# Performance work log

Measured on AMD Instinct MI355X. Metric: run time of the kernel, lower is better.

The kernel has to match this reference:

```python
import jax, jax.numpy as jnp
import numpy as np
import math

_PI = math.pi

@jax.custom_vjp
def atan_spike(h):
    # Heaviside forward, ATan surrogate (alpha=2.0) backward
    return (h >= 0).astype(h.dtype)

def _atan_fwd(h):
    return (h >= 0).astype(h.dtype), h

def _atan_bwd(h, g):
    # d/dh [ (1/pi) atan(pi*h) + 1/2 ] = 1 / (1 + (pi*h)^2)
    return (g / (1.0 + (_PI * h) ** 2),)

atan_spike.defvjp(_atan_fwd, _atan_bwd)

def plif_scan(x, alpha, v_th):
    # x: [T, ...]; PLIF: v += alpha*(x - v); spike; hard reset to 0
    a = alpha.reshape(())
    def step(v, xt):
        v = v + a * (xt - v)
        s = atan_spike(v - v_th)
        v = v * (1.0 - s)
        return v, s
    v0 = jnp.zeros_like(x[0])
    _, spikes = jax.lax.scan(step, v0, x)
    return spikes

def setup_inputs() -> dict:
    key = jax.random.key(0)
    k1, k2, k3 = jax.random.split(key, 3)
    T, B, N, D, H = 4, 8, 1024, 512, 2048
    x = jax.random.normal(k1, (T, B, N, D), dtype=jnp.float32)
    W1 = jax.random.normal(k2, (H, D), dtype=jnp.float32) * (1.0 / math.sqrt(D))
    W2 = jax.random.normal(k3, (D, H), dtype=jnp.float32) * (1.0 / math.sqrt(H))
    alpha1 = jnp.full((1,), 0.5, dtype=jnp.float32)  # 1/tau, tau=2.0
    alpha2 = jnp.full((1,), 0.5, dtype=jnp.float32)
    return {"x": x, "W1": W1, "W2": W2, "alpha1": alpha1, "alpha2": alpha2}

def reference(x, W1, W2, alpha1, alpha2):
    V_TH = 1.0
    h = jnp.einsum('tbnd,hd->tbnh', x, W1)      # fc1 (no bias)
    s1 = plif_scan(h, alpha1, V_TH)             # PLIF neuron 1
    y = jnp.einsum('tbnh,dh->tbnd', s1, W2)     # fc2 (no bias)
    s2 = plif_scan(y, alpha2, V_TH)             # PLIF neuron 2
    return s2
```

## Files before the change

### kernel.cpp

```cpp
#include <hip/hip_runtime.h>

#define T_  4
#define BN_ 8192
#define D_  512
#define H_  2048

typedef float f4 __attribute__((ext_vector_type(4)));
typedef float f32x4 __attribute__((ext_vector_type(4)));
typedef _Float16 f16x8 __attribute__((ext_vector_type(8)));

__device__ __forceinline__ void split8(const f4 u0, const f4 u1, f16x8& hi, f16x8& lo) {
#pragma unroll
    for (int i = 0; i < 4; ++i) {
        _Float16 a = (_Float16)u0[i]; hi[i]     = a; lo[i]     = (_Float16)(u0[i] - (float)a);
        _Float16 b = (_Float16)u1[i]; hi[4 + i] = b; lo[4 + i] = (_Float16)(u1[i] - (float)b);
    }
}

__device__ __forceinline__ void spikes4_to_f16(unsigned b, unsigned& lo, unsigned& hi) {
    const unsigned p0 = (b & 0xFFu) | ((b & 0xFF00u) << 8);
    const unsigned p1 = ((b >> 16) & 0xFFu) | ((b >> 8) & 0xFF0000u);
    lo = p0 * 0x3C00u;
    hi = p1 * 0x3C00u;
}

__device__ __forceinline__ void glds16(const void* g, void* l) {
    __builtin_amdgcn_global_load_lds((const __attribute__((address_space(1))) unsigned int*)g,
                                     (__attribute__((address_space(3))) unsigned int*)l, 16, 0, 0);
}

__global__ __launch_bounds__(256)
void k_split(const float* __restrict__ x, _Float16* __restrict__ xs)
{
    const int b   = blockIdx.x;
    const int t   = b & 3;
    const int k0B = (b >> 2) & 15;
    const int bnB = b >> 6;
    const int kg  = threadIdx.x & 3;
    const int row = threadIdx.x >> 2;

    const float* src = x + ((size_t)t * BN_ + bnB * 64 + row) * D_ + k0B * 32 + kg * 8;
    const f4 u0 = *(const f4*)src;
    const f4 u1 = *(const f4*)(src + 4);
    f16x8 hi, lo;
    split8(u0, u1, hi, lo);

    const size_t base = ((size_t)(bnB * 16 + k0B) * 4 + t) * 4096;
    *(f16x8*)&xs[base +        kg * 512 + row * 8] = hi;
    *(f16x8*)&xs[base + 2048 + kg * 512 + row * 8] = lo;
}

__global__ __launch_bounds__(256)
void k_splitW(const float* __restrict__ W1, _Float16* __restrict__ w1s)
{
    const int gid = blockIdx.x * 256 + threadIdx.x;
    const int col = gid & 127;
    const int kg  = (gid >> 7) & 3;
    const int kb  = (gid >> 9) & 15;
    const int h0b = gid >> 13;

    const float* src = W1 + (size_t)(h0b * 128 + col) * D_ + kb * 32 + kg * 8;
    const f4 u0 = *(const f4*)src;
    const f4 u1 = *(const f4*)(src + 4);
    f16x8 hi, lo;
    split8(u0, u1, hi, lo);

    const size_t base = (size_t)(h0b * 16 + kb) * 8192;
    *(f16x8*)&w1s[base +        kg * 1024 + col * 8] = hi;
    *(f16x8*)&w1s[base + 4096 + kg * 1024 + col * 8] = lo;
}

__global__ __launch_bounds__(256, 2)
void k_fc1b(const _Float16* __restrict__ xs, const _Float16* __restrict__ w1s,
            const float* __restrict__ alphap, unsigned char* __restrict__ s1)
{
    __shared__ _Float16 Ab[2][T_][2][4][64][8];

    const int tid  = threadIdx.x;
    const int lane = tid & 63;
    const int w    = tid >> 6;
    const int wr   = (w >> 1) * 32;
    const int wc   = (w & 1) * 64;
    const int bnB  = blockIdx.x;
    const int bn0  = bnB * 64;
    const int h0   = blockIdx.y * 128;

    const int l15 = lane & 15;
    const int kgl = lane >> 4;
    const int lq  = kgl * 4;

    const float a1v = alphap[0];

    f32x4 acc[T_][2][4];
#pragma unroll
    for (int t = 0; t < T_; ++t)
#pragma unroll
        for (int m = 0; m < 2; ++m)
#pragma unroll
            for (int n = 0; n < 4; ++n) acc[t][m][n] = (f32x4){0.f, 0.f, 0.f, 0.f};

    const char* xbase = (const char*)xs + (size_t)bnB * 16 * 32768;
    const _Float16* bl = w1s + (size_t)blockIdx.y * (16 * 8192)
                             + (size_t)kgl * 1024 + (size_t)(wc + l15) * 8;

    f16x8 bc[2][4], bn_[2][4];

    {
        _Float16* lA = &Ab[0][0][0][0][0][0];
#pragma unroll
        for (int i = 0; i < 8; ++i) {
            const int c = i * 4 + w;
            glds16(xbase + c * 1024 + lane * 16, lA + c * 512);
        }
#pragma unroll
        for (int sp = 0; sp < 2; ++sp)
#pragma unroll
            for (int n = 0; n < 4; ++n)
                bc[sp][n] = *(const f16x8*)(bl + sp * 4096 + n * 128);
    }
    __syncthreads();

    int buf = 0;
    for (int kb = 0; kb < 16; ++kb) {
        if (kb < 15) {
            const char* cb = xbase + (size_t)(kb + 1) * 32768;
            _Float16* lA = &Ab[buf ^ 1][0][0][0][0][0];
#pragma unroll
            for (int i = 0; i < 8; ++i) {
                const int c = i * 4 + w;
                glds16(cb + c * 1024 + lane * 16, lA + c * 512);
            }
            const _Float16* bp = bl + (size_t)(kb + 1) * 8192;
#pragma unroll
            for (int sp = 0; sp < 2; ++sp)
#pragma unroll
                for (int n = 0; n < 4; ++n)
                    bn_[sp][n] = *(const f16x8*)(bp + sp * 4096 + n * 128);
        }

#pragma unroll
        for (int t = 0; t < T_; ++t)
#pragma unroll
            for (int m = 0; m < 2; ++m) {
                const f16x8 a0 = *(const f16x8*)&Ab[buf][t][0][kgl][wr + m * 16 + l15][0];
                const f16x8 a1 = *(const f16x8*)&Ab[buf][t][1][kgl][wr + m * 16 + l15][0];
#pragma unroll
                for (int n = 0; n < 4; ++n) {
                    acc[t][m][n] = __builtin_amdgcn_mfma_f32_16x16x32_f16(a0, bc[0][n], acc[t][m][n], 0, 0, 0);
                    acc[t][m][n] = __builtin_amdgcn_mfma_f32_16x16x32_f16(a0, bc[1][n], acc[t][m][n], 0, 0, 0);
                    acc[t][m][n] = __builtin_amdgcn_mfma_f32_16x16x32_f16(a1, bc[0][n], acc[t][m][n], 0, 0, 0);
                }
            }

        __syncthreads();
        if (kb < 15) {
#pragma unroll
            for (int sp = 0; sp < 2; ++sp)
#pragma unroll
                for (int n = 0; n < 4; ++n) bc[sp][n] = bn_[sp][n];
        }
        buf ^= 1;
    }

#pragma unroll
    for (int m = 0; m < 2; ++m)
#pragma unroll
        for (int n = 0; n < 4; ++n)
#pragma unroll
            for (int q = 0; q < 4; ++q) {
                float v = 0.f;
#pragma unroll
                for (int t = 0; t < T_; ++t) {
                    v = v + a1v * (acc[t][m][n][q] - v);
                    const bool sp = (v >= 1.0f);
                    s1[((size_t)t * BN_ + bn0 + wr + m * 16 + lq + q) * H_ +
                       (h0 + wc + n * 16 + l15)] = sp ? (unsigned char)1 : (unsigned char)0;
                    if (sp) v = 0.f;
                }
            }
}

__global__ __launch_bounds__(256, 2)
void k_fc1(const _Float16* __restrict__ xs, const float* __restrict__ W1,
           const float* __restrict__ alphap, unsigned char* __restrict__ s1)
{
    __shared__ _Float16 Ab[T_][2][4][64][8];
    __shared__ _Float16 Bb[2][4][128][8];

    const int tid  = threadIdx.x;
    const int lane = tid & 63;
    const int w    = tid >> 6;
    const int wr   = (w >> 1) * 32;
    const int wc   = (w & 1) * 64;
    const int bnB  = blockIdx.x;
    const int bn0  = bnB * 64;
    const int h0   = blockIdx.y * 128;

    const int l15 = lane & 15;
    const int kgl = lane >> 4;
    const int lq  = kgl * 4;

    const int bcol = tid & 127;
    const int bkh  = tid >> 7;

    const float a1v = alphap[0];

    f32x4 acc[T_][2][4];
#pragma unroll
    for (int t = 0; t < T_; ++t)
#pragma unroll
        for (int m = 0; m < 2; ++m)
#pragma unroll
            for (int n = 0; n < 4; ++n) acc[t][m][n] = (f32x4){0.f, 0.f, 0.f, 0.f};

    const char* xbase = (const char*)xs + (size_t)bnB * 16 * 32768;
    const float* wp0  = W1 + (size_t)(h0 + bcol) * D_ + bkh * 16;

    f4 w0 = *(const f4*)wp0,       w1 = *(const f4*)(wp0 + 4);
    f4 w2 = *(const f4*)(wp0 + 8), w3 = *(const f4*)(wp0 + 12);

    for (int kb = 0; kb < 16; ++kb) {
        __syncthreads();
        const char* cb = xbase + (size_t)kb * 32768;
        _Float16* lA = &Ab[0][0][0][0][0];
#pragma unroll
        for (int i = 0; i < 8; ++i) {
            const int c = i * 4 + w;
            glds16(cb + c * 1024 + lane * 16, lA + c * 512);
        }
        {
            f16x8 hA, lA2, hB, lB;
            split8(w0, w1, hA, lA2); split8(w2, w3, hB, lB);
            *(f16x8*)&Bb[0][2 * bkh][bcol][0]     = hA;
            *(f16x8*)&Bb[0][2 * bkh + 1][bcol][0] = hB;
            *(f16x8*)&Bb[1][2 * bkh][bcol][0]     = lA2;
            *(f16x8*)&Bb[1][2 * bkh + 1][bcol][0] = lB;
        }
        if (kb < 15) {
            const float* wp = wp0 + (kb + 1) * 32;
            w0 = *(const f4*)wp;       w1 = *(const f4*)(wp + 4);
            w2 = *(const f4*)(wp + 8); w3 = *(const f4*)(wp + 12);
        }
        __syncthreads();

        f16x8 bf0[4], bf1[4];
#pragma unroll
        for (int n = 0; n < 4; ++n) {
            bf0[n] = *(const f16x8*)&Bb[0][kgl][wc + n * 16 + l15][0];
            bf1[n] = *(const f16x8*)&Bb[1][kgl][wc + n * 16 + l15][0];
        }
#pragma unroll
        for (int t = 0; t < T_; ++t)
#pragma unroll
            for (int m = 0; m < 2; ++m) {
                const f16x8 a0 = *(const f16x8*)&Ab[t][0][kgl][wr + m * 16 + l15][0];
                const f16x8 a1 = *(const f16x8*)&Ab[t][1][kgl][wr + m * 16 + l15][0];
#pragma unroll
                for (int n = 0; n < 4; ++n) {
                    acc[t][m][n] = __builtin_amdgcn_mfma_f32_16x16x32_f16(a0, bf0[n], acc[t][m][n], 0, 0, 0);
                    acc[t][m][n] = __builtin_amdgcn_mfma_f32_16x16x32_f16(a0, bf1[n], acc[t][m][n], 0, 0, 0);
                    acc[t][m][n] = __builtin_amdgcn_mfma_f32_16x16x32_f16(a1, bf0[n], acc[t][m][n], 0, 0, 0);
                }
            }
    }

#pragma unroll
    for (int m = 0; m < 2; ++m)
#pragma unroll
        for (int n = 0; n < 4; ++n)
#pragma unroll
            for (int q = 0; q < 4; ++q) {
                float v = 0.f;
#pragma unroll
                for (int t = 0; t < T_; ++t) {
                    v = v + a1v * (acc[t][m][n][q] - v);
                    const bool sp = (v >= 1.0f);
                    s1[((size_t)t * BN_ + bn0 + wr + m * 16 + lq + q) * H_ +
                       (h0 + wc + n * 16 + l15)] = sp ? (unsigned char)1 : (unsigned char)0;
                    if (sp) v = 0.f;
                }
            }
}

__global__ __launch_bounds__(256, 2)
void k_fc2(const unsigned char* __restrict__ s1, const float* __restrict__ W2,
           const float* __restrict__ alphap, float* __restrict__ out)
{
    __shared__ _Float16 A2[2][4][4][64][8];
    __shared__ _Float16 B2[2][2][4][128][8];

    const int tid  = threadIdx.x;
    const int lane = tid & 63;
    const int w    = tid >> 6;
    const int wr   = (w >> 1) * 32;
    const int wc   = (w & 1) * 64;
    const int bn0  = blockIdx.x * 64;
    const int d0   = blockIdx.y * 128;

    const int l15 = lane & 15;
    const int kgl = lane >> 4;
    const int lq  = kgl * 4;

    const int bcol = tid & 127;
    const int bkh  = tid >> 7;
    const int at   = tid >> 6;
    const int arow = lane;

    const float a2v = alphap[0];

    f32x4 acc[T_][2][4];
#pragma unroll
    for (int t = 0; t < T_; ++t)
#pragma unroll
        for (int m = 0; m < 2; ++m)
#pragma unroll
            for (int n = 0; n < 4; ++n) acc[t][m][n] = (f32x4){0.f, 0.f, 0.f, 0.f};

    const unsigned char* ap = s1 + ((size_t)at * BN_ + bn0 + arow) * H_;
    const float*         wp0 = W2 + (size_t)(d0 + bcol) * H_ + bkh * 16;

    {
        const uint4 r0 = *(const uint4*)(ap);
        const uint4 r1 = *(const uint4*)(ap + 16);
        unsigned v[8];
        spikes4_to_f16(r0.x, v[0], v[1]); spikes4_to_f16(r0.y, v[2], v[3]);
        spikes4_to_f16(r0.z, v[4], v[5]); spikes4_to_f16(r0.w, v[6], v[7]);
        *(uint4*)&A2[0][at][0][arow][0] = *(const uint4*)&v[0];
        *(uint4*)&A2[0][at][1][arow][0] = *(const uint4*)&v[4];
        spikes4_to_f16(r1.x, v[0], v[1]); spikes4_to_f16(r1.y, v[2], v[3]);
        spikes4_to_f16(r1.z, v[4], v[5]); spikes4_to_f16(r1.w, v[6], v[7]);
        *(uint4*)&A2[0][at][2][arow][0] = *(const uint4*)&v[0];
        *(uint4*)&A2[0][at][3][arow][0] = *(const uint4*)&v[4];

        const f4 w0 = *(const f4*)wp0, w1 = *(const f4*)(wp0 + 4);
        const f4 w2 = *(const f4*)(wp0 + 8), w3 = *(const f4*)(wp0 + 12);
        f16x8 hA, lA, hB, lB;
        split8(w0, w1, hA, lA); split8(w2, w3, hB, lB);
        *(f16x8*)&B2[0][0][2 * bkh][bcol][0]     = hA;
        *(f16x8*)&B2[0][0][2 * bkh + 1][bcol][0] = hB;
        *(f16x8*)&B2[0][1][2 * bkh][bcol][0]     = lA;
        *(f16x8*)&B2[0][1][2 * bkh + 1][bcol][0] = lB;
    }
    __syncthreads();

    int cur = 0;
    for (int kb = 0; kb < 64; ++kb) {
        uint4 r0, r1; f4 w0, w1, w2, w3;
        if (kb < 63) {
            r0 = *(const uint4*)(ap + (kb + 1) * 32);
            r1 = *(const uint4*)(ap + (kb + 1) * 32 + 16);
            const float* wp = wp0 + (kb + 1) * 32;
            w0 = *(const f4*)wp;       w1 = *(const f4*)(wp + 4);
            w2 = *(const f4*)(wp + 8); w3 = *(const f4*)(wp + 12);
        }

        f16x8 bf0[4], bf1[4];
#pragma unroll
        for (int n = 0; n < 4; ++n) {
            bf0[n] = *(const f16x8*)&B2[cur][0][kgl][wc + n * 16 + l15][0];
            bf1[n] = *(const f16x8*)&B2[cur][1][kgl][wc + n * 16 + l15][0];
        }
#pragma unroll
        for (int t = 0; t < T_; ++t)
#pragma unroll
            for (int m = 0; m < 2; ++m) {
                const f16x8 af = *(const f16x8*)&A2[cur][t][kgl][wr + m * 16 + l15][0];
#pragma unroll
                for (int n = 0; n < 4; ++n) {
                    acc[t][m][n] = __builtin_amdgcn_mfma_f32_16x16x32_f16(af, bf0[n], acc[t][m][n], 0, 0, 0);
                    acc[t][m][n] = __builtin_amdgcn_mfma_f32_16x16x32_f16(af, bf1[n], acc[t][m][n], 0, 0, 0);
                }
            }

        if (kb < 63) {
            unsigned v[8];
            spikes4_to_f16(r0.x, v[0], v[1]); spikes4_to_f16(r0.y, v[2], v[3]);
            spikes4_to_f16(r0.z, v[4], v[5]); spikes4_to_f16(r0.w, v[6], v[7]);
            *(uint4*)&A2[cur ^ 1][at][0][arow][0] = *(const uint4*)&v[0];
            *(uint4*)&A2[cur ^ 1][at][1][arow][0] = *(const uint4*)&v[4];
            spikes4_to_f16(r1.x, v[0], v[1]); spikes4_to_f16(r1.y, v[2], v[3]);
            spikes4_to_f16(r1.z, v[4], v[5]); spikes4_to_f16(r1.w, v[6], v[7]);
            *(uint4*)&A2[cur ^ 1][at][2][arow][0] = *(const uint4*)&v[0];
            *(uint4*)&A2[cur ^ 1][at][3][arow][0] = *(const uint4*)&v[4];

            f16x8 hA, lA, hB, lB;
            split8(w0, w1, hA, lA); split8(w2, w3, hB, lB);
            *(f16x8*)&B2[cur ^ 1][0][2 * bkh][bcol][0]     = hA;
            *(f16x8*)&B2[cur ^ 1][0][2 * bkh + 1][bcol][0] = hB;
            *(f16x8*)&B2[cur ^ 1][1][2 * bkh][bcol][0]     = lA;
            *(f16x8*)&B2[cur ^ 1][1][2 * bkh + 1][bcol][0] = lB;
        }
        __syncthreads();
        cur ^= 1;
    }

#pragma unroll
    for (int m = 0; m < 2; ++m)
#pragma unroll
        for (int n = 0; n < 4; ++n)
#pragma unroll
            for (int q = 0; q < 4; ++q) {
                float v = 0.f;
#pragma unroll
                for (int t = 0; t < T_; ++t) {
                    v = v + a2v * (acc[t][m][n][q] - v);
                    const bool sp = (v >= 1.0f);
                    out[((size_t)t * BN_ + bn0 + wr + m * 16 + lq + q) * D_ +
                        (d0 + wc + n * 16 + l15)] = sp ? 1.0f : 0.0f;
                    if (sp) v = 0.f;
                }
            }
}

extern "C" void kernel_launch(void* const* d_in, const int* in_sizes, int n_in,
                              void* d_out, int out_size, void* d_ws, size_t ws_size,
                              hipStream_t stream) {
    const float* x      = (const float*)d_in[0];
    const float* W1     = (const float*)d_in[1];
    const float* W2     = (const float*)d_in[2];
    const float* alpha1 = (const float*)d_in[3];
    const float* alpha2 = (const float*)d_in[4];
    float* out = (float*)d_out;

    unsigned char* s1 = (unsigned char*)d_ws;
    _Float16* xs = (_Float16*)d_out;
    const size_t S1_BYTES = (size_t)T_ * BN_ * H_;
    const size_t W1S_BYTES = (size_t)H_ * D_ * 2 * sizeof(_Float16);

    k_split<<<dim3(8192), dim3(256), 0, stream>>>(x, xs);

    if (ws_size >= S1_BYTES + W1S_BYTES) {
        _Float16* w1s = (_Float16*)((char*)d_ws + S1_BYTES);
        k_splitW<<<dim3(512), dim3(256), 0, stream>>>(W1, w1s);
        k_fc1b<<<dim3(128, 16), dim3(256), 0, stream>>>(xs, w1s, alpha1, s1);
    } else {
        k_fc1<<<dim3(128, 16), dim3(256), 0, stream>>>(xs, W1, alpha1, s1);
    }
    k_fc2<<<dim3(128, 4), dim3(256), 0, stream>>>(s1, W2, alpha2, out);
}
```

Baseline: 304.8 us.

## Swizzle fc1 block order into panels and unroll K loop by two

Launches fc1 as a 1D grid and remaps each block id so that 16 row-blocks sweep all 16 H-tiles inside a 256-block panel. Nearby blocks then share x and W1 tiles in L2. The K loop is also manually unrolled by two with ping-pong register buffers for B, which removes the per-iteration register copy and the buffer-index toggling. The remap assumes exactly 2048 blocks laid out this way.

```diff
diff --git a/kernel.cpp b/kernel.cpp
--- a/kernel.cpp
+++ b/kernel.cpp
@@ -81,9 +81,14 @@
     const int w    = tid >> 6;
     const int wr   = (w >> 1) * 32;
     const int wc   = (w & 1) * 64;
-    const int bnB  = blockIdx.x;
-    const int bn0  = bnB * 64;
-    const int h0   = blockIdx.y * 128;
+
+    const int gid   = blockIdx.x;
+    const int panel = gid >> 8;
+    const int h0i   = (gid >> 4) & 15;
+    const int bnL   = gid & 15;
+    const int bnB   = panel * 16 + bnL;
+    const int bn0   = bnB * 64;
+    const int h0    = h0i * 128;
 
     const int l15 = lane & 15;
     const int kgl = lane >> 4;
@@ -100,66 +105,64 @@
             for (int n = 0; n < 4; ++n) acc[t][m][n] = (f32x4){0.f, 0.f, 0.f, 0.f};
 
     const char* xbase = (const char*)xs + (size_t)bnB * 16 * 32768;
-    const _Float16* bl = w1s + (size_t)blockIdx.y * (16 * 8192)
+    const _Float16* bl = w1s + (size_t)h0i * (16 * 8192)
                              + (size_t)kgl * 1024 + (size_t)(wc + l15) * 8;
 
-    f16x8 bc[2][4], bn_[2][4];
-
-    {
-        _Float16* lA = &Ab[0][0][0][0][0][0];
-#pragma unroll
-        for (int i = 0; i < 8; ++i) {
-            const int c = i * 4 + w;
-            glds16(xbase + c * 1024 + lane * 16, lA + c * 512);
-        }
-#pragma unroll
-        for (int sp = 0; sp < 2; ++sp)
-#pragma unroll
-            for (int n = 0; n < 4; ++n)
-                bc[sp][n] = *(const f16x8*)(bl + sp * 4096 + n * 128);
-    }
+#define FC1_GLDS(BUF, KB)                                                        \
+    {                                                                            \
+        const char* cb_ = xbase + (size_t)(KB) * 32768;                          \
+        _Float16* lA_ = &Ab[BUF][0][0][0][0][0];                                 \
+        _Pragma("unroll")                                                        \
+        for (int i_ = 0; i_ < 8; ++i_) {                                         \
+            const int c_ = i_ * 4 + w;                                           \
+            glds16(cb_ + c_ * 1024 + lane * 16, lA_ + c_ * 512);                 \
+        }                                                                        \
+    }
+
+#define FC1_BLOAD(KB, B0, B1)                                                    \
+    {                                                                            \
+        const _Float16* bp_ = bl + (size_t)(KB) * 8192;                          \
+        _Pragma("unroll")                                                        \
+        for (int n_ = 0; n_ < 4; ++n_) {                                         \
+            B0[n_] = *(const f16x8*)(bp_ + n_ * 128);                            \
+            B1[n_] = *(const f16x8*)(bp_ + 4096 + n_ * 128);                     \
+        }                                                                        \
+    }
+
+#define FC1_COMPUTE(BUF, B0, B1)                                                 \
+    _Pragma("unroll")                                                            \
+    for (int t_ = 0; t_ < T_; ++t_)                                              \
+        _Pragma("unroll")                                                        \
+        for (int m_ = 0; m_ < 2; ++m_) {                                         \
+            const f16x8 a0_ = *(const f16x8*)&Ab[BUF][t_][0][kgl][wr + m_ * 16 + l15][0]; \
+            const f16x8 a1_ = *(const f16x8*)&Ab[BUF][t_][1][kgl][wr + m_ * 16 + l15][0]; \
+            _Pragma("unroll")                                                    \
+            for (int n_ = 0; n_ < 4; ++n_) {                                     \
+                acc[t_][m_][n_] = __builtin_amdgcn_mfma_f32_16x16x32_f16(a0_, B0[n_], acc[t_][m_][n_], 0, 0, 0); \
+                acc[t_][m_][n_] = __builtin_amdgcn_mfma_f32_16x16x32_f16(a0_, B1[n_], acc[t_][m_][n_], 0, 0, 0); \
+                acc[t_][m_][n_] = __builtin_amdgcn_mfma_f32_16x16x32_f16(a1_, B0[n_], acc[t_][m_][n_], 0, 0, 0); \
+            }                                                                    \
+        }
+
+    f16x8 bA0[4], bA1[4], bB0[4], bB1[4];
+
+    FC1_GLDS(0, 0)
+    FC1_BLOAD(0, bA0, bA1)
     __syncthreads();
 
-    int buf = 0;
-    for (int kb = 0; kb < 16; ++kb) {
-        if (kb < 15) {
-            const char* cb = xbase + (size_t)(kb + 1) * 32768;
-            _Float16* lA = &Ab[buf ^ 1][0][0][0][0][0];
-#pragma unroll
-            for (int i = 0; i < 8; ++i) {
-                const int c = i * 4 + w;
-                glds16(cb + c * 1024 + lane * 16, lA + c * 512);
-            }
-            const _Float16* bp = bl + (size_t)(kb + 1) * 8192;
-#pragma unroll
-            for (int sp = 0; sp < 2; ++sp)
-#pragma unroll
-                for (int n = 0; n < 4; ++n)
-                    bn_[sp][n] = *(const f16x8*)(bp + sp * 4096 + n * 128);
-        }
-
-#pragma unroll
-        for (int t = 0; t < T_; ++t)
-#pragma unroll
-            for (int m = 0; m < 2; ++m) {
-                const f16x8 a0 = *(const f16x8*)&Ab[buf][t][0][kgl][wr + m * 16 + l15][0];
-                const f16x8 a1 = *(const f16x8*)&Ab[buf][t][1][kgl][wr + m * 16 + l15][0];
-#pragma unroll
-                for (int n = 0; n < 4; ++n) {
-                    acc[t][m][n] = __builtin_amdgcn_mfma_f32_16x16x32_f16(a0, bc[0][n], acc[t][m][n], 0, 0, 0);
-                    acc[t][m][n] = __builtin_amdgcn_mfma_f32_16x16x32_f16(a0, bc[1][n], acc[t][m][n], 0, 0, 0);
-                    acc[t][m][n] = __builtin_amdgcn_mfma_f32_16x16x32_f16(a1, bc[0][n], acc[t][m][n], 0, 0, 0);
-                }
-            }
-
+#pragma unroll 1
+    for (int it = 0; it < 8; ++it) {
+        const int kb = 2 * it;
+        FC1_GLDS(1, kb + 1)
+        FC1_BLOAD(kb + 1, bB0, bB1)
+        FC1_COMPUTE(0, bA0, bA1)
         __syncthreads();
-        if (kb < 15) {
-#pragma unroll
-            for (int sp = 0; sp < 2; ++sp)
-#pragma unroll
-                for (int n = 0; n < 4; ++n) bc[sp][n] = bn_[sp][n];
-        }
-        buf ^= 1;
+        if (it < 7) {
+            FC1_GLDS(0, kb + 2)
+            FC1_BLOAD(kb + 2, bA0, bA1)
+        }
+        FC1_COMPUTE(1, bB0, bB1)
+        __syncthreads();
     }
 
 #pragma unroll
@@ -432,7 +435,7 @@
     if (ws_size >= S1_BYTES + W1S_BYTES) {
         _Float16* w1s = (_Float16*)((char*)d_ws + S1_BYTES);
         k_splitW<<<dim3(512), dim3(256), 0, stream>>>(W1, w1s);
-        k_fc1b<<<dim3(128, 16), dim3(256), 0, stream>>>(xs, w1s, alpha1, s1);
+        k_fc1b<<<dim3(2048), dim3(256), 0, stream>>>(xs, w1s, alpha1, s1);
     } else {
         k_fc1<<<dim3(128, 16), dim3(256), 0, stream>>>(xs, W1, alpha1, s1);
     }
```

Result: no change. 310.0 us (+1.7%).
